# Performance work log

Hardware: AMD Instinct MI355X
Metric: run time of the kernel (lower is better)

The kernel has to match this reference:

```python
import jax, jax.numpy as jnp
import numpy as np

N = 4000      # number_of_sensors
D_IN = 128    # input feature dim
D_OUT = 128   # output feature dim
E_DIM = 16    # node embedding dim
B = 8         # batch size


def setup_inputs() -> dict:
    key = jax.random.key(0)
    k_x, k_e1, k_e2, k_w = jax.random.split(key, 4)
    x = jax.random.normal(k_x, (B, N, D_IN), dtype=jnp.float32)
    E1 = jax.random.normal(k_e1, (N, E_DIM), dtype=jnp.float32)
    E2 = jax.random.normal(k_e2, (N, E_DIM), dtype=jnp.float32)
    W = jax.random.normal(k_w, (D_IN, D_OUT), dtype=jnp.float32) * (1.0 / np.sqrt(D_IN))
    b = jnp.zeros((D_OUT,), dtype=jnp.float32)
    return {"x": x, "E1": E1, "E2": E2, "W": W, "b": b}


def reference(x, E1, E2, W, b):
    # Adaptive adjacency from node embeddings: A = softmax(relu(E1 @ E2^T), axis=-1)
    logits = jax.nn.relu(jnp.einsum('nd,md->nm', E1, E2))  # [N, N]
    adj = jax.nn.softmax(logits, axis=-1)                  # row-normalized adjacency
    # Graph aggregation then feature transform: relu(A @ X @ W + b)
    agg = jnp.einsum('nm,bmf->bnf', adj, x)                # [B, N, D_IN]
    out = jax.nn.relu(jnp.einsum('bnf,fo->bno', agg, W) + b)  # [B, N, D_OUT]
    return out
```

## Files before the change

kernel.cpp:

```cpp
#include <hip/hip_runtime.h>
#include <hip/hip_bf16.h>

#define NSEN 4000
#define NP   4096
#define DIN  128
#define DOUT 128
#define EDIM 16
#define BATCH 8

typedef __attribute__((ext_vector_type(8))) short bf16x8;
typedef __attribute__((ext_vector_type(4))) float f32x4;

__device__ __forceinline__ unsigned short f2bf(float f) {
  unsigned int u = __float_as_uint(f);
  unsigned int r = (u + 0x7FFFu + ((u >> 16) & 1u)) >> 16;
  return (unsigned short)r;
}
__device__ __forceinline__ float bf2f(unsigned short s) {
  unsigned int u = ((unsigned int)s) << 16;
  return __uint_as_float(u);
}

__device__ __forceinline__ void gl_lds16(const void* g, void* l) {
  __builtin_amdgcn_global_load_lds((const __attribute__((address_space(1))) void*)g,
                                   (__attribute__((address_space(3))) void*)l, 16, 0, 0);
}

__global__ __launch_bounds__(512) void k_prep(const float* __restrict__ E1,
                                              const float* __restrict__ E2,
                                              const float* __restrict__ W,
                                              const float* __restrict__ x,
                                              unsigned short* __restrict__ adjp,
                                              float* __restrict__ rinv,
                                              unsigned short* __restrict__ yt) {
  __shared__ float rsum[8][16];
  __shared__ __align__(16) unsigned short pool[34816];
  const int bx = blockIdx.x;
  const int tid = threadIdx.x;
  const int lane = tid & 63, wv = tid >> 6;
  const int lr = lane & 15, lq = lane >> 4;

  if (bx >= 250) {
    unsigned short* wlds = pool;
    unsigned short* ylds = pool + 17408;
    {
      const int fr = tid >> 5;
      const int o4 = tid & 31;
#pragma unroll
      for (int r8 = 0; r8 < 8; r8++) {
        const int f = fr + r8 * 16;
        float4 w4 = *(const float4*)&W[(size_t)f * DOUT + o4 * 4];
        wlds[(o4 * 4 + 0) * 136 + f] = f2bf(w4.x);
        wlds[(o4 * 4 + 1) * 136 + f] = f2bf(w4.y);
        wlds[(o4 * 4 + 2) * 136 + f] = f2bf(w4.z);
        wlds[(o4 * 4 + 3) * 136 + f] = f2bf(w4.w);
      }
    }
    __syncthreads();

    const int yi = bx - 250;
    const int b  = yi >> 5;
    const int m0 = (yi & 31) * 128;
    const int mh = wv >> 2;
    const int os = wv & 3;

    bf16x8 af[2][4];
#pragma unroll
    for (int ot = 0; ot < 2; ot++) {
      const int ob = os * 32 + ot * 16 + lr;
#pragma unroll
      for (int ks = 0; ks < 4; ks++)
        af[ot][ks] = *(const bf16x8*)&wlds[ob * 136 + ks * 32 + lq * 8];
    }

#pragma unroll
    for (int mt = 0; mt < 4; mt++) {
      const int mloc = mh * 64 + mt * 16;
      const int m = m0 + mloc + lr;
      bf16x8 bx8[4];
      if (m < NSEN) {
        const float* xp = &x[((size_t)b * NSEN + m) * DIN + lq * 8];
#pragma unroll
        for (int ks = 0; ks < 4; ks++) {
          float4 v0 = *(const float4*)(xp + ks * 32);
          float4 v1 = *(const float4*)(xp + ks * 32 + 4);
          bx8[ks][0] = (short)f2bf(v0.x); bx8[ks][1] = (short)f2bf(v0.y);
          bx8[ks][2] = (short)f2bf(v0.z); bx8[ks][3] = (short)f2bf(v0.w);
          bx8[ks][4] = (short)f2bf(v1.x); bx8[ks][5] = (short)f2bf(v1.y);
          bx8[ks][6] = (short)f2bf(v1.z); bx8[ks][7] = (short)f2bf(v1.w);
        }
      } else {
#pragma unroll
        for (int ks = 0; ks < 4; ks++)
#pragma unroll
          for (int j = 0; j < 8; j++) bx8[ks][j] = 0;
      }
#pragma unroll
      for (int ot = 0; ot < 2; ot++) {
        f32x4 c = (f32x4){0.f, 0.f, 0.f, 0.f};
#pragma unroll
        for (int ks = 0; ks < 4; ks++)
          c = __builtin_amdgcn_mfma_f32_16x16x32_bf16(af[ot][ks], bx8[ks], c, 0, 0, 0);
#pragma unroll
        for (int i = 0; i < 4; i++)
          ylds[(os * 32 + ot * 16 + lq * 4 + i) * 136 + mloc + lr] = f2bf(c[i]);
      }
    }
    __syncthreads();
#pragma unroll
    for (int s2 = 0; s2 < 4; s2++) {
      int c = s2 * 512 + tid;
      int row = c >> 4;
      int mc = c & 15;
      *(bf16x8*)&yt[(size_t)(b * 128 + row) * NP + m0 + mc * 8] =
          *(const bf16x8*)&ylds[row * 136 + mc * 8];
    }
    return;
  }

  unsigned short* bounce = pool;
  const int n0 = bx * 16;

  float a[8];
  {
    const float* e1p = &E1[(size_t)(n0 + lr) * EDIM + (lq & 1) * 8];
    *(float4*)&a[0] = *(const float4*)e1p;
    *(float4*)&a[4] = *(const float4*)(e1p + 4);
  }
  bf16x8 af1, af2;
#pragma unroll
  for (int j = 0; j < 8; j++) {
    unsigned short hs = f2bf(a[j]);
    af1[j] = (short)hs;
    float lo = a[j] - bf2f(hs);
    af2[j] = (lq < 2) ? (short)f2bf(lo) : (short)0;
  }

  float rs[4] = {0.f, 0.f, 0.f, 0.f};
  for (int w0 = 0; w0 < 256; w0 += 64) {
    if (w0 == 192) {
      for (int z = tid; z < 16 * 96; z += 512) {
        int zr = z / 96, zc = z % 96;
        bounce[zr * 1040 + 58 * 16 + zc] = 0;
      }
    }
    const int tend = (w0 + 64 < 250) ? (w0 + 64) : 250;
    for (int t = w0 + wv; t < tend; t += 8) {
      const int m = t * 16 + lr;
      float bv[8];
      const float* e2p = &E2[(size_t)m * EDIM + (lq & 1) * 8];
      *(float4*)&bv[0] = *(const float4*)e2p;
      *(float4*)&bv[4] = *(const float4*)(e2p + 4);
      bf16x8 bfrag;
#pragma unroll
      for (int j = 0; j < 8; j++) {
        unsigned short hs = f2bf(bv[j]);
        if (lq < 2) bfrag[j] = (short)hs;
        else        bfrag[j] = (short)f2bf(bv[j] - bf2f(hs));
      }
      f32x4 c = (f32x4){0.f, 0.f, 0.f, 0.f};
      c = __builtin_amdgcn_mfma_f32_16x16x32_bf16(af1, bfrag, c, 0, 0, 0);
      c = __builtin_amdgcn_mfma_f32_16x16x32_bf16(af2, bfrag, c, 0, 0, 0);
#pragma unroll
      for (int i = 0; i < 4; i++) {
        float p = __expf(fmaxf(c[i], 0.f));
        rs[i] += p;
        bounce[(lq * 4 + i) * 1040 + (t - w0) * 16 + lr] = f2bf(p);
      }
    }
    __syncthreads();
#pragma unroll
    for (int s2 = 0; s2 < 4; s2++) {
      int cch = s2 * 512 + tid;
      int row = cch >> 7, mc = cch & 127;
      *(bf16x8*)&adjp[(size_t)(n0 + row) * NP + w0 * 16 + mc * 8] =
          *(const bf16x8*)&bounce[row * 1040 + mc * 8];
    }
    __syncthreads();
  }
#pragma unroll
  for (int i = 0; i < 4; i++) {
    rs[i] += __shfl_xor(rs[i], 1, 64);
    rs[i] += __shfl_xor(rs[i], 2, 64);
    rs[i] += __shfl_xor(rs[i], 4, 64);
    rs[i] += __shfl_xor(rs[i], 8, 64);
  }
  if (lr == 0) {
#pragma unroll
    for (int i = 0; i < 4; i++) rsum[wv][lq * 4 + i] = rs[i];
  }
  __syncthreads();
  if (tid < 16) {
    float s = 0.f;
#pragma unroll
    for (int w = 0; w < 8; w++) s += rsum[w][tid];
    rinv[n0 + tid] = 1.0f / s;
  }
}

__global__ __launch_bounds__(512, 2) void k_gemm(const unsigned short* __restrict__ A,
                                                 const unsigned short* __restrict__ Bt,
                                                 unsigned short* __restrict__ part,
                                                 int nsteps) {
  __shared__ __align__(16) unsigned short smem[65536];
  unsigned short* tA0 = smem;
  unsigned short* tB0 = smem + 32768;
  const int tid = threadIdx.x;
  const int lane = tid & 63, wv = tid >> 6;
  const int wr = wv >> 2, wcn = wv & 3;
  const int lr = lane & 15, lq = lane >> 4;
  const int kh = blockIdx.x >> 4;
  const int m0 = (blockIdx.x & 15) * 256;
  const int n0c = blockIdx.y * 256;
  const int kb0 = kh * nsteps * 64;

  f32x4 acc[8][4];
#pragma unroll
  for (int p = 0; p < 8; p++)
#pragma unroll
    for (int q = 0; q < 4; q++) acc[p][q] = (f32x4){0.f, 0.f, 0.f, 0.f};

#define STAGE(bufi, kb)                                                                 \
  {                                                                                     \
    _Pragma("unroll")                                                                   \
    for (int s = 0; s < 4; s++) {                                                       \
      int idx = s * 512 + tid;                                                          \
      int row = idx >> 3;                                                               \
      int kc = ((idx & 7) ^ (row & 7)) << 3;                                            \
      gl_lds16(&A[(size_t)(m0 + row) * NP + (kb) + kc], &tA0[(bufi)*16384 + idx*8]);    \
      gl_lds16(&Bt[(size_t)(n0c + row) * NP + (kb) + kc], &tB0[(bufi)*16384 + idx*8]);  \
    }                                                                                   \
  }

  STAGE(0, kb0);

  for (int it = 0; it < nsteps; ++it) {
    const int cur = it & 1;
    if (it < nsteps - 1) {
      STAGE(cur ^ 1, kb0 + (it + 1) * 64);
      asm volatile("s_waitcnt vmcnt(8)" ::: "memory");
    } else {
      asm volatile("s_waitcnt vmcnt(0)" ::: "memory");
    }
    __builtin_amdgcn_s_barrier();

    {
      const int koff = (lq * 8) ^ ((lr & 7) << 3);
      bf16x8 af[8], bf[4];
#pragma unroll
      for (int p = 0; p < 8; p++)
        af[p] = *(const bf16x8*)&tA0[cur * 16384 + (wr * 128 + p * 16 + lr) * 64 + koff];
#pragma unroll
      for (int q = 0; q < 4; q++)
        bf[q] = *(const bf16x8*)&tB0[cur * 16384 + (wcn * 64 + q * 16 + lr) * 64 + koff];
      asm volatile("s_waitcnt lgkmcnt(0)" ::: "memory");
      __builtin_amdgcn_sched_barrier(0);
      __builtin_amdgcn_s_setprio(1);
#pragma unroll
      for (int p = 0; p < 8; p++)
#pragma unroll
        for (int q = 0; q < 4; q++)
          acc[p][q] = __builtin_amdgcn_mfma_f32_16x16x32_bf16(af[p], bf[q], acc[p][q], 0, 0, 0);
      __builtin_amdgcn_s_setprio(0);
    }
    {
      const int koff = (32 + lq * 8) ^ ((lr & 7) << 3);
      bf16x8 af[8], bf[4];
#pragma unroll
      for (int p = 0; p < 8; p++)
        af[p] = *(const bf16x8*)&tA0[cur * 16384 + (wr * 128 + p * 16 + lr) * 64 + koff];
#pragma unroll
      for (int q = 0; q < 4; q++)
        bf[q] = *(const bf16x8*)&tB0[cur * 16384 + (wcn * 64 + q * 16 + lr) * 64 + koff];
      asm volatile("s_waitcnt lgkmcnt(0)" ::: "memory");
      __builtin_amdgcn_sched_barrier(0);
      __builtin_amdgcn_s_setprio(1);
#pragma unroll
      for (int p = 0; p < 8; p++)
#pragma unroll
        for (int q = 0; q < 4; q++)
          acc[p][q] = __builtin_amdgcn_mfma_f32_16x16x32_bf16(af[p], bf[q], acc[p][q], 0, 0, 0);
      __builtin_amdgcn_s_setprio(0);
    }
    __builtin_amdgcn_s_barrier();
  }
#undef STAGE

  unsigned short* pdst = part + ((size_t)kh << 22);
#pragma unroll
  for (int p = 0; p < 8; p++)
#pragma unroll
    for (int q = 0; q < 4; q++) {
      const int col = n0c + wcn * 64 + q * 16 + lr;
#pragma unroll
      for (int i = 0; i < 4; i++) {
        const int row = m0 + wr * 128 + p * 16 + lq * 4 + i;
        pdst[(size_t)row * 1024 + col] = f2bf(acc[p][q][i]);
      }
    }
}

__global__ __launch_bounds__(256) void k_fin(const unsigned short* __restrict__ part,
                                             const float* __restrict__ rinv,
                                             const float* __restrict__ bias,
                                             float* __restrict__ out, int ksl) {
  const int tid = threadIdx.x;
  const int nl = tid >> 4;
  const int ch = tid & 15;
  const int n  = blockIdx.x * 16 + nl;
  const int b  = blockIdx.y;
  const int j  = b * 128 + ch * 8;

  float s[8] = {0.f, 0.f, 0.f, 0.f, 0.f, 0.f, 0.f, 0.f};
  for (int kh = 0; kh < ksl; kh++) {
    bf16x8 pv = *(const bf16x8*)&part[((size_t)kh << 22) + (size_t)n * 1024 + j];
#pragma unroll
    for (int jj = 0; jj < 8; jj++) s[jj] += bf2f((unsigned short)pv[jj]);
  }
  const float rv = rinv[n];
  float4 bb0 = *(const float4*)&bias[ch * 8];
  float4 bb1 = *(const float4*)&bias[ch * 8 + 4];
  float r[8];
#pragma unroll
  for (int jj = 0; jj < 8; jj++) {
    float bbj = (jj < 4) ? ((const float*)&bb0)[jj] : ((const float*)&bb1)[jj - 4];
    r[jj] = fmaxf(s[jj] * rv + bbj, 0.f);
  }
  float* op = &out[((size_t)b * NSEN + n) * DOUT + ch * 8];
  *(float4*)op       = make_float4(r[0], r[1], r[2], r[3]);
  *(float4*)(op + 4) = make_float4(r[4], r[5], r[6], r[7]);
}

extern "C" void kernel_launch(void* const* d_in, const int* in_sizes, int n_in,
                              void* d_out, int out_size, void* d_ws, size_t ws_size,
                              hipStream_t stream) {
  const float* x    = (const float*)d_in[0];
  const float* E1   = (const float*)d_in[1];
  const float* E2   = (const float*)d_in[2];
  const float* W    = (const float*)d_in[3];
  const float* bias = (const float*)d_in[4];
  float* out = (float*)d_out;

  char* ws = (char*)d_ws;
  unsigned short* adjp = (unsigned short*)(ws);
  unsigned short* yt   = (unsigned short*)(ws + 33554432);
  float*          rinv = (float*)(ws + 33554432 + 8388608);
  unsigned short* part = (unsigned short*)(ws + 33554432 + 8388608 + 16384);

  const size_t need4 = 33554432ull + 8388608 + 16384 + 4ull * 8388608;
  const int KS = (ws_size >= need4) ? 4 : 2;
  const int nsteps = 64 / KS;

  k_prep<<<dim3(506), dim3(512), 0, stream>>>(E1, E2, W, x, adjp, rinv, yt);
  k_gemm<<<dim3(KS * 16, 4), dim3(512), 0, stream>>>(adjp, yt, part, nsteps);
  k_fin<<<dim3(250, BATCH), dim3(256), 0, stream>>>(part, rinv, bias, out, KS);
}
```

Measured before the change: 81.75 us.

## Interleave prefetch with MFMA sub-phases in GEMM and write adjacency directly

The GEMM main loop is split into four half-tile MFMA phases. Each phase issues one quarter of the next tile's global-to-LDS loads and waits with a finer vmcnt, so loads overlap compute in a ping-pong style with extra barriers. The adjacency builder drops the LDS bounce buffer and per-chunk syncs, storing bf16 values straight to global and zeroing the padding columns separately. The direct stores are narrow 2-byte scattered writes, which may coalesce worse than the earlier 16-byte staged stores. The added barriers also raise sync overhead.

```diff
diff --git a/kernel.cpp b/kernel.cpp
--- a/kernel.cpp
+++ b/kernel.cpp
@@ -118,7 +118,6 @@
     return;
   }
 
-  unsigned short* bounce = pool;
   const int n0 = bx * 16;
 
   float a[8];
@@ -137,46 +136,32 @@
   }
 
   float rs[4] = {0.f, 0.f, 0.f, 0.f};
-  for (int w0 = 0; w0 < 256; w0 += 64) {
-    if (w0 == 192) {
-      for (int z = tid; z < 16 * 96; z += 512) {
-        int zr = z / 96, zc = z % 96;
-        bounce[zr * 1040 + 58 * 16 + zc] = 0;
-      }
-    }
-    const int tend = (w0 + 64 < 250) ? (w0 + 64) : 250;
-    for (int t = w0 + wv; t < tend; t += 8) {
-      const int m = t * 16 + lr;
-      float bv[8];
-      const float* e2p = &E2[(size_t)m * EDIM + (lq & 1) * 8];
-      *(float4*)&bv[0] = *(const float4*)e2p;
-      *(float4*)&bv[4] = *(const float4*)(e2p + 4);
-      bf16x8 bfrag;
-#pragma unroll
-      for (int j = 0; j < 8; j++) {
-        unsigned short hs = f2bf(bv[j]);
-        if (lq < 2) bfrag[j] = (short)hs;
-        else        bfrag[j] = (short)f2bf(bv[j] - bf2f(hs));
-      }
-      f32x4 c = (f32x4){0.f, 0.f, 0.f, 0.f};
-      c = __builtin_amdgcn_mfma_f32_16x16x32_bf16(af1, bfrag, c, 0, 0, 0);
-      c = __builtin_amdgcn_mfma_f32_16x16x32_bf16(af2, bfrag, c, 0, 0, 0);
-#pragma unroll
-      for (int i = 0; i < 4; i++) {
-        float p = __expf(fmaxf(c[i], 0.f));
-        rs[i] += p;
-        bounce[(lq * 4 + i) * 1040 + (t - w0) * 16 + lr] = f2bf(p);
-      }
-    }
-    __syncthreads();
-#pragma unroll
-    for (int s2 = 0; s2 < 4; s2++) {
-      int cch = s2 * 512 + tid;
-      int row = cch >> 7, mc = cch & 127;
-      *(bf16x8*)&adjp[(size_t)(n0 + row) * NP + w0 * 16 + mc * 8] =
-          *(const bf16x8*)&bounce[row * 1040 + mc * 8];
-    }
-    __syncthreads();
+  for (int t = wv; t < NSEN / 16; t += 8) {
+    const int m = t * 16 + lr;
+    float bv[8];
+    const float* e2p = &E2[(size_t)m * EDIM + (lq & 1) * 8];
+    *(float4*)&bv[0] = *(const float4*)e2p;
+    *(float4*)&bv[4] = *(const float4*)(e2p + 4);
+    bf16x8 bfrag;
+#pragma unroll
+    for (int j = 0; j < 8; j++) {
+      unsigned short hs = f2bf(bv[j]);
+      if (lq < 2) bfrag[j] = (short)hs;
+      else        bfrag[j] = (short)f2bf(bv[j] - bf2f(hs));
+    }
+    f32x4 c = (f32x4){0.f, 0.f, 0.f, 0.f};
+    c = __builtin_amdgcn_mfma_f32_16x16x32_bf16(af1, bfrag, c, 0, 0, 0);
+    c = __builtin_amdgcn_mfma_f32_16x16x32_bf16(af2, bfrag, c, 0, 0, 0);
+#pragma unroll
+    for (int i = 0; i < 4; i++) {
+      float p = __expf(fmaxf(c[i], 0.f));
+      rs[i] += p;
+      adjp[(size_t)(n0 + lq * 4 + i) * NP + t * 16 + lr] = f2bf(p);
+    }
+  }
+  for (int i = tid; i < 16 * (NP - NSEN); i += 512) {
+    int r = i / (NP - NSEN), c = i % (NP - NSEN);
+    adjp[(size_t)(n0 + r) * NP + NSEN + c] = 0;
   }
 #pragma unroll
   for (int i = 0; i < 4; i++) {
@@ -220,71 +205,78 @@
 #pragma unroll
     for (int q = 0; q < 4; q++) acc[p][q] = (f32x4){0.f, 0.f, 0.f, 0.f};
 
-#define STAGE(bufi, kb)                                                                 \
+#define STAGE2(bufi, kb, s)                                                             \
   {                                                                                     \
-    _Pragma("unroll")                                                                   \
-    for (int s = 0; s < 4; s++) {                                                       \
-      int idx = s * 512 + tid;                                                          \
-      int row = idx >> 3;                                                               \
-      int kc = ((idx & 7) ^ (row & 7)) << 3;                                            \
-      gl_lds16(&A[(size_t)(m0 + row) * NP + (kb) + kc], &tA0[(bufi)*16384 + idx*8]);    \
-      gl_lds16(&Bt[(size_t)(n0c + row) * NP + (kb) + kc], &tB0[(bufi)*16384 + idx*8]);  \
-    }                                                                                   \
-  }
-
-  STAGE(0, kb0);
+    int idx = (s) * 512 + tid;                                                          \
+    int row = idx >> 3;                                                                 \
+    int kc = ((idx & 7) ^ (row & 7)) << 3;                                              \
+    gl_lds16(&A[(size_t)(m0 + row) * NP + (kb) + kc], &tA0[(bufi)*16384 + idx*8]);      \
+    gl_lds16(&Bt[(size_t)(n0c + row) * NP + (kb) + kc], &tB0[(bufi)*16384 + idx*8]);    \
+  }
+
+  STAGE2(0, kb0, 0); STAGE2(0, kb0, 1); STAGE2(0, kb0, 2); STAGE2(0, kb0, 3);
 
   for (int it = 0; it < nsteps; ++it) {
     const int cur = it & 1;
-    if (it < nsteps - 1) {
-      STAGE(cur ^ 1, kb0 + (it + 1) * 64);
-      asm volatile("s_waitcnt vmcnt(8)" ::: "memory");
-    } else {
-      asm volatile("s_waitcnt vmcnt(0)" ::: "memory");
-    }
-    __builtin_amdgcn_s_barrier();
-
-    {
-      const int koff = (lq * 8) ^ ((lr & 7) << 3);
-      bf16x8 af[8], bf[4];
-#pragma unroll
-      for (int p = 0; p < 8; p++)
-        af[p] = *(const bf16x8*)&tA0[cur * 16384 + (wr * 128 + p * 16 + lr) * 64 + koff];
-#pragma unroll
-      for (int q = 0; q < 4; q++)
-        bf[q] = *(const bf16x8*)&tB0[cur * 16384 + (wcn * 64 + q * 16 + lr) * 64 + koff];
-      asm volatile("s_waitcnt lgkmcnt(0)" ::: "memory");
-      __builtin_amdgcn_sched_barrier(0);
-      __builtin_amdgcn_s_setprio(1);
-#pragma unroll
-      for (int p = 0; p < 8; p++)
+    const int nxt = cur ^ 1;
+    const int kbn = kb0 + (it + 1) * 64;
+    const bool pf = (it < nsteps - 1);
+    bf16x8 bf[4];
+
+#pragma unroll
+    for (int ks = 0; ks < 2; ks++) {
+      if (ks == 0) {
+        if (pf) STAGE2(nxt, kbn, 0);
+        if (it == 0) { asm volatile("s_waitcnt vmcnt(0)" ::: "memory"); }
+        else if (pf) { asm volatile("s_waitcnt vmcnt(2)" ::: "memory"); }
+        else         { asm volatile("s_waitcnt vmcnt(0)" ::: "memory"); }
+        __builtin_amdgcn_s_barrier();
+      } else {
+        if (pf) STAGE2(nxt, kbn, 2);
+      }
+      {
+        const int koff = (ks * 32 + lq * 8) ^ ((lr & 7) << 3);
+        bf16x8 af[4];
+#pragma unroll
+        for (int p = 0; p < 4; p++)
+          af[p] = *(const bf16x8*)&tA0[cur * 16384 + (wr * 128 + p * 16 + lr) * 64 + koff];
 #pragma unroll
         for (int q = 0; q < 4; q++)
-          acc[p][q] = __builtin_amdgcn_mfma_f32_16x16x32_bf16(af[p], bf[q], acc[p][q], 0, 0, 0);
-      __builtin_amdgcn_s_setprio(0);
-    }
-    {
-      const int koff = (32 + lq * 8) ^ ((lr & 7) << 3);
-      bf16x8 af[8], bf[4];
-#pragma unroll
-      for (int p = 0; p < 8; p++)
-        af[p] = *(const bf16x8*)&tA0[cur * 16384 + (wr * 128 + p * 16 + lr) * 64 + koff];
-#pragma unroll
-      for (int q = 0; q < 4; q++)
-        bf[q] = *(const bf16x8*)&tB0[cur * 16384 + (wcn * 64 + q * 16 + lr) * 64 + koff];
-      asm volatile("s_waitcnt lgkmcnt(0)" ::: "memory");
-      __builtin_amdgcn_sched_barrier(0);
-      __builtin_amdgcn_s_setprio(1);
-#pragma unroll
-      for (int p = 0; p < 8; p++)
-#pragma unroll
-        for (int q = 0; q < 4; q++)
-          acc[p][q] = __builtin_amdgcn_mfma_f32_16x16x32_bf16(af[p], bf[q], acc[p][q], 0, 0, 0);
-      __builtin_amdgcn_s_setprio(0);
-    }
-    __builtin_amdgcn_s_barrier();
-  }
-#undef STAGE
+          bf[q] = *(const bf16x8*)&tB0[cur * 16384 + (wcn * 64 + q * 16 + lr) * 64 + koff];
+        if (ks == 1) __builtin_amdgcn_s_barrier();
+        asm volatile("s_waitcnt lgkmcnt(0)" ::: "memory");
+        __builtin_amdgcn_sched_barrier(0);
+        __builtin_amdgcn_s_setprio(1);
+#pragma unroll
+        for (int p = 0; p < 4; p++)
+#pragma unroll
+          for (int q = 0; q < 4; q++)
+            acc[p][q] = __builtin_amdgcn_mfma_f32_16x16x32_bf16(af[p], bf[q], acc[p][q], 0, 0, 0);
+        __builtin_amdgcn_s_setprio(0);
+        __builtin_amdgcn_s_barrier();
+      }
+      {
+        if (pf) STAGE2(nxt, kbn, (ks == 0) ? 1 : 3);
+        const int koff = (ks * 32 + lq * 8) ^ ((lr & 7) << 3);
+        bf16x8 af[4];
+#pragma unroll
+        for (int p = 0; p < 4; p++)
+          af[p] = *(const bf16x8*)&tA0[cur * 16384 + (wr * 128 + (4 + p) * 16 + lr) * 64 + koff];
+        __builtin_amdgcn_s_barrier();
+        asm volatile("s_waitcnt lgkmcnt(0)" ::: "memory");
+        __builtin_amdgcn_sched_barrier(0);
+        __builtin_amdgcn_s_setprio(1);
+#pragma unroll
+        for (int p = 0; p < 4; p++)
+#pragma unroll
+          for (int q = 0; q < 4; q++)
+            acc[4 + p][q] = __builtin_amdgcn_mfma_f32_16x16x32_bf16(af[p], bf[q], acc[4 + p][q], 0, 0, 0);
+        __builtin_amdgcn_s_setprio(0);
+        __builtin_amdgcn_s_barrier();
+      }
+    }
+  }
+#undef STAGE2
 
   unsigned short* pdst = part + ((size_t)kh << 22);
 #pragma unroll
```

New measurement: 79.28 us. 1.03x faster.

## Generate adjacency tiles on the fly inside the GEMM instead of materializing them

Applied to the files above, without the earlier changes.

Stops writing the full 4096x4096 bf16 exp-adjacency matrix to global memory. The GEMM kernel now computes each A tile directly in LDS from split hi/lo bf16 embeddings using MFMA plus exp, and accumulates partial row sums that the finalize kernel reduces. This removes about 32 MB of write and read traffic and shortens the prep kernel. In exchange the GEMM main loop does extra MFMA and exp work, and the recompute is repeated across the 4 column blocks.

```diff
diff --git a/kernel.cpp b/kernel.cpp
--- a/kernel.cpp
+++ b/kernel.cpp
@@ -26,181 +26,118 @@
                                    (__attribute__((address_space(3))) void*)l, 16, 0, 0);
 }
 
-__global__ __launch_bounds__(512) void k_prep(const float* __restrict__ E1,
+__global__ __launch_bounds__(512) void k_prep(const float* __restrict__ W,
+                                              const float* __restrict__ x,
+                                              const float* __restrict__ E1,
                                               const float* __restrict__ E2,
-                                              const float* __restrict__ W,
-                                              const float* __restrict__ x,
-                                              unsigned short* __restrict__ adjp,
-                                              float* __restrict__ rinv,
-                                              unsigned short* __restrict__ yt) {
-  __shared__ float rsum[8][16];
-  __shared__ __align__(16) unsigned short pool[34816];
+                                              unsigned short* __restrict__ yt,
+                                              unsigned short* __restrict__ e1h,
+                                              unsigned short* __restrict__ e1l,
+                                              unsigned short* __restrict__ e2h,
+                                              unsigned short* __restrict__ e2l) {
   const int bx = blockIdx.x;
   const int tid = threadIdx.x;
+
+  if (bx >= 256) {
+    for (int i = (bx - 256) * 512 + tid; i < NP * EDIM; i += 8 * 512) {
+      float v1 = (i < NSEN * EDIM) ? E1[i] : 0.f;
+      unsigned short h1 = f2bf(v1);
+      e1h[i] = h1;
+      e1l[i] = f2bf(v1 - bf2f(h1));
+      float v2 = (i < NSEN * EDIM) ? E2[i] : 0.f;
+      unsigned short h2 = f2bf(v2);
+      e2h[i] = h2;
+      e2l[i] = f2bf(v2 - bf2f(h2));
+    }
+    return;
+  }
+
+  __shared__ __align__(16) unsigned short pool[34816];
+  unsigned short* wlds = pool;
+  unsigned short* ylds = pool + 17408;
   const int lane = tid & 63, wv = tid >> 6;
   const int lr = lane & 15, lq = lane >> 4;
 
-  if (bx >= 250) {
-    unsigned short* wlds = pool;
-    unsigned short* ylds = pool + 17408;
-    {
-      const int fr = tid >> 5;
-      const int o4 = tid & 31;
-#pragma unroll
-      for (int r8 = 0; r8 < 8; r8++) {
-        const int f = fr + r8 * 16;
-        float4 w4 = *(const float4*)&W[(size_t)f * DOUT + o4 * 4];
-        wlds[(o4 * 4 + 0) * 136 + f] = f2bf(w4.x);
-        wlds[(o4 * 4 + 1) * 136 + f] = f2bf(w4.y);
-        wlds[(o4 * 4 + 2) * 136 + f] = f2bf(w4.z);
-        wlds[(o4 * 4 + 3) * 136 + f] = f2bf(w4.w);
+  {
+    const int fr = tid >> 5;
+    const int o4 = tid & 31;
+#pragma unroll
+    for (int r8 = 0; r8 < 8; r8++) {
+      const int f = fr + r8 * 16;
+      float4 w4 = *(const float4*)&W[(size_t)f * DOUT + o4 * 4];
+      wlds[(o4 * 4 + 0) * 136 + f] = f2bf(w4.x);
+      wlds[(o4 * 4 + 1) * 136 + f] = f2bf(w4.y);
+      wlds[(o4 * 4 + 2) * 136 + f] = f2bf(w4.z);
+      wlds[(o4 * 4 + 3) * 136 + f] = f2bf(w4.w);
+    }
+  }
+  __syncthreads();
+
+  const int b  = bx >> 5;
+  const int m0 = (bx & 31) * 128;
+  const int mh = wv >> 2;
+  const int os = wv & 3;
+
+  bf16x8 af[2][4];
+#pragma unroll
+  for (int ot = 0; ot < 2; ot++) {
+    const int ob = os * 32 + ot * 16 + lr;
+#pragma unroll
+    for (int ks = 0; ks < 4; ks++)
+      af[ot][ks] = *(const bf16x8*)&wlds[ob * 136 + ks * 32 + lq * 8];
+  }
+
+#pragma unroll
+  for (int mt = 0; mt < 4; mt++) {
+    const int mloc = mh * 64 + mt * 16;
+    const int m = m0 + mloc + lr;
+    bf16x8 bx8[4];
+    if (m < NSEN) {
+      const float* xp = &x[((size_t)b * NSEN + m) * DIN + lq * 8];
+#pragma unroll
+      for (int ks = 0; ks < 4; ks++) {
+        float4 v0 = *(const float4*)(xp + ks * 32);
+        float4 v1 = *(const float4*)(xp + ks * 32 + 4);
+        bx8[ks][0] = (short)f2bf(v0.x); bx8[ks][1] = (short)f2bf(v0.y);
+        bx8[ks][2] = (short)f2bf(v0.z); bx8[ks][3] = (short)f2bf(v0.w);
+        bx8[ks][4] = (short)f2bf(v1.x); bx8[ks][5] = (short)f2bf(v1.y);
+        bx8[ks][6] = (short)f2bf(v1.z); bx8[ks][7] = (short)f2bf(v1.w);
       }
-    }
-    __syncthreads();
-
-    const int yi = bx - 250;
-    const int b  = yi >> 5;
-    const int m0 = (yi & 31) * 128;
-    const int mh = wv >> 2;
-    const int os = wv & 3;
-
-    bf16x8 af[2][4];
+    } else {
+#pragma unroll
+      for (int ks = 0; ks < 4; ks++)
+#pragma unroll
+        for (int j = 0; j < 8; j++) bx8[ks][j] = 0;
+    }
 #pragma unroll
     for (int ot = 0; ot < 2; ot++) {
-      const int ob = os * 32 + ot * 16 + lr;
+      f32x4 c = (f32x4){0.f, 0.f, 0.f, 0.f};
 #pragma unroll
       for (int ks = 0; ks < 4; ks++)
-        af[ot][ks] = *(const bf16x8*)&wlds[ob * 136 + ks * 32 + lq * 8];
-    }
-
-#pragma unroll
-    for (int mt = 0; mt < 4; mt++) {
-      const int mloc = mh * 64 + mt * 16;
-      const int m = m0 + mloc + lr;
-      bf16x8 bx8[4];
-      if (m < NSEN) {
-        const float* xp = &x[((size_t)b * NSEN + m) * DIN + lq * 8];
-#pragma unroll
-        for (int ks = 0; ks < 4; ks++) {
-          float4 v0 = *(const float4*)(xp + ks * 32);
-          float4 v1 = *(const float4*)(xp + ks * 32 + 4);
-          bx8[ks][0] = (short)f2bf(v0.x); bx8[ks][1] = (short)f2bf(v0.y);
-          bx8[ks][2] = (short)f2bf(v0.z); bx8[ks][3] = (short)f2bf(v0.w);
-          bx8[ks][4] = (short)f2bf(v1.x); bx8[ks][5] = (short)f2bf(v1.y);
-          bx8[ks][6] = (short)f2bf(v1.z); bx8[ks][7] = (short)f2bf(v1.w);
-        }
-      } else {
-#pragma unroll
-        for (int ks = 0; ks < 4; ks++)
-#pragma unroll
-          for (int j = 0; j < 8; j++) bx8[ks][j] = 0;
-      }
-#pragma unroll
-      for (int ot = 0; ot < 2; ot++) {
-        f32x4 c = (f32x4){0.f, 0.f, 0.f, 0.f};
-#pragma unroll
-        for (int ks = 0; ks < 4; ks++)
-          c = __builtin_amdgcn_mfma_f32_16x16x32_bf16(af[ot][ks], bx8[ks], c, 0, 0, 0);
-#pragma unroll
-        for (int i = 0; i < 4; i++)
-          ylds[(os * 32 + ot * 16 + lq * 4 + i) * 136 + mloc + lr] = f2bf(c[i]);
-      }
-    }
-    __syncthreads();
-#pragma unroll
-    for (int s2 = 0; s2 < 4; s2++) {
-      int c = s2 * 512 + tid;
-      int row = c >> 4;
-      int mc = c & 15;
-      *(bf16x8*)&yt[(size_t)(b * 128 + row) * NP + m0 + mc * 8] =
-          *(const bf16x8*)&ylds[row * 136 + mc * 8];
-    }
-    return;
-  }
-
-  unsigned short* bounce = pool;
-  const int n0 = bx * 16;
-
-  float a[8];
-  {
-    const float* e1p = &E1[(size_t)(n0 + lr) * EDIM + (lq & 1) * 8];
-    *(float4*)&a[0] = *(const float4*)e1p;
-    *(float4*)&a[4] = *(const float4*)(e1p + 4);
-  }
-  bf16x8 af1, af2;
-#pragma unroll
-  for (int j = 0; j < 8; j++) {
-    unsigned short hs = f2bf(a[j]);
-    af1[j] = (short)hs;
-    float lo = a[j] - bf2f(hs);
-    af2[j] = (lq < 2) ? (short)f2bf(lo) : (short)0;
-  }
-
-  float rs[4] = {0.f, 0.f, 0.f, 0.f};
-  for (int w0 = 0; w0 < 256; w0 += 64) {
-    if (w0 == 192) {
-      for (int z = tid; z < 16 * 96; z += 512) {
-        int zr = z / 96, zc = z % 96;
-        bounce[zr * 1040 + 58 * 16 + zc] = 0;
-      }
-    }
-    const int tend = (w0 + 64 < 250) ? (w0 + 64) : 250;
-    for (int t = w0 + wv; t < tend; t += 8) {
-      const int m = t * 16 + lr;
-      float bv[8];
-      const float* e2p = &E2[(size_t)m * EDIM + (lq & 1) * 8];
-      *(float4*)&bv[0] = *(const float4*)e2p;
-      *(float4*)&bv[4] = *(const float4*)(e2p + 4);
-      bf16x8 bfrag;
-#pragma unroll
-      for (int j = 0; j < 8; j++) {
-        unsigned short hs = f2bf(bv[j]);
-        if (lq < 2) bfrag[j] = (short)hs;
-        else        bfrag[j] = (short)f2bf(bv[j] - bf2f(hs));
-      }
-      f32x4 c = (f32x4){0.f, 0.f, 0.f, 0.f};
-      c = __builtin_amdgcn_mfma_f32_16x16x32_bf16(af1, bfrag, c, 0, 0, 0);
-      c = __builtin_amdgcn_mfma_f32_16x16x32_bf16(af2, bfrag, c, 0, 0, 0);
-#pragma unroll
-      for (int i = 0; i < 4; i++) {
-        float p = __expf(fmaxf(c[i], 0.f));
-        rs[i] += p;
-        bounce[(lq * 4 + i) * 1040 + (t - w0) * 16 + lr] = f2bf(p);
-      }
-    }
-    __syncthreads();
-#pragma unroll
-    for (int s2 = 0; s2 < 4; s2++) {
-      int cch = s2 * 512 + tid;
-      int row = cch >> 7, mc = cch & 127;
-      *(bf16x8*)&adjp[(size_t)(n0 + row) * NP + w0 * 16 + mc * 8] =
-          *(const bf16x8*)&bounce[row * 1040 + mc * 8];
-    }
-    __syncthreads();
-  }
-#pragma unroll
-  for (int i = 0; i < 4; i++) {
-    rs[i] += __shfl_xor(rs[i], 1, 64);
-    rs[i] += __shfl_xor(rs[i], 2, 64);
-    rs[i] += __shfl_xor(rs[i], 4, 64);
-    rs[i] += __shfl_xor(rs[i], 8, 64);
-  }
-  if (lr == 0) {
-#pragma unroll
-    for (int i = 0; i < 4; i++) rsum[wv][lq * 4 + i] = rs[i];
+        c = __builtin_amdgcn_mfma_f32_16x16x32_bf16(af[ot][ks], bx8[ks], c, 0, 0, 0);
+#pragma unroll
+      for (int i = 0; i < 4; i++)
+        ylds[(os * 32 + ot * 16 + lq * 4 + i) * 136 + mloc + lr] = f2bf(c[i]);
+    }
   }
   __syncthreads();
-  if (tid < 16) {
-    float s = 0.f;
-#pragma unroll
-    for (int w = 0; w < 8; w++) s += rsum[w][tid];
-    rinv[n0 + tid] = 1.0f / s;
-  }
-}
-
-__global__ __launch_bounds__(512, 2) void k_gemm(const unsigned short* __restrict__ A,
+#pragma unroll
+  for (int s2 = 0; s2 < 4; s2++) {
+    int c = s2 * 512 + tid;
+    int row = c >> 4;
+    int mc = c & 15;
+    *(bf16x8*)&yt[(size_t)(b * 128 + row) * NP + m0 + mc * 8] =
+        *(const bf16x8*)&ylds[row * 136 + mc * 8];
+  }
+}
+
+__global__ __launch_bounds__(512, 2) void k_gemm(const unsigned short* __restrict__ e1h,
+                                                 const unsigned short* __restrict__ e1l,
+                                                 const unsigned short* __restrict__ e2h,
+                                                 const unsigned short* __restrict__ e2l,
                                                  const unsigned short* __restrict__ Bt,
                                                  unsigned short* __restrict__ part,
+                                                 float* __restrict__ rowsumP,
                                                  int nsteps) {
   __shared__ __align__(16) unsigned short smem[65536];
   unsigned short* tA0 = smem;
@@ -209,36 +146,82 @@
   const int lane = tid & 63, wv = tid >> 6;
   const int wr = wv >> 2, wcn = wv & 3;
   const int lr = lane & 15, lq = lane >> 4;
-  const int kh = blockIdx.x >> 4;
-  const int m0 = (blockIdx.x & 15) * 256;
+  const int kh = blockIdx.x & 3;
+  const int m0 = (blockIdx.x >> 2) * 256;
   const int n0c = blockIdx.y * 256;
   const int kb0 = kh * nsteps * 64;
 
+  bf16x8 e1f[2];
+#pragma unroll
+  for (int mt = 0; mt < 2; mt++) {
+    const size_t m = m0 + wv * 32 + mt * 16 + lr;
+    e1f[mt] = (lq < 2) ? *(const bf16x8*)&e1h[m * EDIM + lq * 8]
+                       : *(const bf16x8*)&e1l[m * EDIM + (lq & 1) * 8];
+  }
+
+  float rsacc[2] = {0.f, 0.f};
+
   f32x4 acc[8][4];
 #pragma unroll
   for (int p = 0; p < 8; p++)
 #pragma unroll
     for (int q = 0; q < 4; q++) acc[p][q] = (f32x4){0.f, 0.f, 0.f, 0.f};
 
-#define STAGE(bufi, kb)                                                                 \
+#define STAGE_B(bufi, kb)                                                               \
   {                                                                                     \
     _Pragma("unroll")                                                                   \
     for (int s = 0; s < 4; s++) {                                                       \
       int idx = s * 512 + tid;                                                          \
       int row = idx >> 3;                                                               \
       int kc = ((idx & 7) ^ (row & 7)) << 3;                                            \
-      gl_lds16(&A[(size_t)(m0 + row) * NP + (kb) + kc], &tA0[(bufi)*16384 + idx*8]);    \
       gl_lds16(&Bt[(size_t)(n0c + row) * NP + (kb) + kc], &tB0[(bufi)*16384 + idx*8]);  \
     }                                                                                   \
   }
 
-  STAGE(0, kb0);
+#define GEN_A(bufi, kb)                                                                 \
+  {                                                                                     \
+    bf16x8 ga1[4], ga2[4];                                                              \
+    _Pragma("unroll")                                                                   \
+    for (int kt = 0; kt < 4; kt++) {                                                    \
+      const size_t kr = (kb) + kt * 16 + lr;                                            \
+      ga1[kt] = *(const bf16x8*)&e2h[kr * EDIM + (lq & 1) * 8];                         \
+      bf16x8 z = {0, 0, 0, 0, 0, 0, 0, 0};                                              \
+      if (lq < 2) z = *(const bf16x8*)&e2l[kr * EDIM + lq * 8];                         \
+      ga2[kt] = z;                                                                      \
+    }                                                                                   \
+    _Pragma("unroll")                                                                   \
+    for (int kt = 0; kt < 4; kt++) {                                                    \
+      _Pragma("unroll")                                                                 \
+      for (int mt = 0; mt < 2; mt++) {                                                  \
+        f32x4 c = (f32x4){0.f, 0.f, 0.f, 0.f};                                          \
+        c = __builtin_amdgcn_mfma_f32_16x16x32_bf16(ga1[kt], e1f[mt], c, 0, 0, 0);      \
+        c = __builtin_amdgcn_mfma_f32_16x16x32_bf16(ga2[kt], e1f[mt], c, 0, 0, 0);      \
+        const int kgb = (kb) + kt * 16 + lq * 4;                                        \
+        float pv[4];                                                                    \
+        _Pragma("unroll")                                                               \
+        for (int i = 0; i < 4; i++)                                                     \
+          pv[i] = (kgb + i < NSEN) ? __expf(fmaxf(c[i], 0.f)) : 0.f;                    \
+        rsacc[mt] += (pv[0] + pv[1]) + (pv[2] + pv[3]);                                 \
+        const int mloc = wv * 32 + mt * 16 + lr;                                        \
+        const int chs = (kt * 2 + (lq >> 1)) ^ (mloc & 7);                              \
+        uint2 w;                                                                        \
+        w.x = (unsigned)f2bf(pv[0]) | ((unsigned)f2bf(pv[1]) << 16);                    \
+        w.y = (unsigned)f2bf(pv[2]) | ((unsigned)f2bf(pv[3]) << 16);                    \
+        *(uint2*)&tA0[(bufi) * 16384 + mloc * 64 + chs * 8 + (lq & 1) * 4] = w;         \
+      }                                                                                 \
+    }                                                                                   \
+  }
+
+  GEN_A(0, kb0);
+  STAGE_B(0, kb0);
+  asm volatile("s_waitcnt lgkmcnt(0)" ::: "memory");
 
   for (int it = 0; it < nsteps; ++it) {
     const int cur = it & 1;
     if (it < nsteps - 1) {
-      STAGE(cur ^ 1, kb0 + (it + 1) * 64);
-      asm volatile("s_waitcnt vmcnt(8)" ::: "memory");
+      GEN_A(cur ^ 1, kb0 + (it + 1) * 64);
+      STAGE_B(cur ^ 1, kb0 + (it + 1) * 64);
+      asm volatile("s_waitcnt vmcnt(4)" ::: "memory");
     } else {
       asm volatile("s_waitcnt vmcnt(0)" ::: "memory");
     }
@@ -284,7 +267,19 @@
     }
     __builtin_amdgcn_s_barrier();
   }
-#undef STAGE
+#undef STAGE_B
+#undef GEN_A
+
+#pragma unroll
+  for (int mt = 0; mt < 2; mt++) {
+    rsacc[mt] += __shfl_xor(rsacc[mt], 16, 64);
+    rsacc[mt] += __shfl_xor(rsacc[mt], 32, 64);
+  }
+  if (blockIdx.y == 0 && lq == 0) {
+#pragma unroll
+    for (int mt = 0; mt < 2; mt++)
+      rowsumP[kh * NP + m0 + wv * 32 + mt * 16 + lr] = rsacc[mt];
+  }
 
   unsigned short* pdst = part + ((size_t)kh << 22);
 #pragma unroll
@@ -301,7 +296,7 @@
 }
 
 __global__ __launch_bounds__(256) void k_fin(const unsigned short* __restrict__ part,
-                                             const float* __restrict__ rinv,
+                                             const float* __restrict__ rowsumP,
                                              const float* __restrict__ bias,
                                              float* __restrict__ out, int ksl) {
   const int tid = threadIdx.x;
@@ -311,13 +306,16 @@
   const int b  = blockIdx.y;
   const int j  = b * 128 + ch * 8;
 
+  float rsum = 0.f;
+  for (int kh = 0; kh < ksl; kh++) rsum += rowsumP[kh * NP + n];
+  const float rv = 1.f / rsum;
+
   float s[8] = {0.f, 0.f, 0.f, 0.f, 0.f, 0.f, 0.f, 0.f};
   for (int kh = 0; kh < ksl; kh++) {
     bf16x8 pv = *(const bf16x8*)&part[((size_t)kh << 22) + (size_t)n * 1024 + j];
 #pragma unroll
     for (int jj = 0; jj < 8; jj++) s[jj] += bf2f((unsigned short)pv[jj]);
   }
-  const float rv = rinv[n];
   float4 bb0 = *(const float4*)&bias[ch * 8];
   float4 bb1 = *(const float4*)&bias[ch * 8 + 4];
   float r[8];
@@ -342,16 +340,17 @@
   float* out = (float*)d_out;
 
   char* ws = (char*)d_ws;
-  unsigned short* adjp = (unsigned short*)(ws);
-  unsigned short* yt   = (unsigned short*)(ws + 33554432);
-  float*          rinv = (float*)(ws + 33554432 + 8388608);
-  unsigned short* part = (unsigned short*)(ws + 33554432 + 8388608 + 16384);
-
-  const size_t need4 = 33554432ull + 8388608 + 16384 + 4ull * 8388608;
-  const int KS = (ws_size >= need4) ? 4 : 2;
-  const int nsteps = 64 / KS;
-
-  k_prep<<<dim3(506), dim3(512), 0, stream>>>(E1, E2, W, x, adjp, rinv, yt);
-  k_gemm<<<dim3(KS * 16, 4), dim3(512), 0, stream>>>(adjp, yt, part, nsteps);
-  k_fin<<<dim3(250, BATCH), dim3(256), 0, stream>>>(part, rinv, bias, out, KS);
-}
+  unsigned short* yt   = (unsigned short*)(ws);
+  unsigned short* e1h  = (unsigned short*)(ws + 8388608);
+  unsigned short* e1l  = (unsigned short*)(ws + 8388608 + 131072);
+  unsigned short* e2h  = (unsigned short*)(ws + 8388608 + 262144);
+  unsigned short* e2l  = (unsigned short*)(ws + 8388608 + 393216);
+  float* rowsumP       = (float*)(ws + 8388608 + 524288);
+  unsigned short* part = (unsigned short*)(ws + 8388608 + 524288 + 65536);
+
+  const int KS = 4, nsteps = 64 / KS;
+
+  k_prep<<<dim3(264), dim3(512), 0, stream>>>(W, x, E1, E2, yt, e1h, e1l, e2h, e2l);
+  k_gemm<<<dim3(KS * 16, 4), dim3(512), 0, stream>>>(e1h, e1l, e2h, e2l, yt, part, rowsumP, nsteps);
+  k_fin<<<dim3(250, BATCH), dim3(256), 0, stream>>>(part, rowsumP, bias, out, KS);
+}
```

New measurement: 98.78 us. 20.8% more time.
